# Performance work log

Measured on AMD Instinct MI355X. Metric: run time of the kernel, lower is better.

The kernel has to match this reference:

```python
import jax, jax.numpy as jnp
import numpy as np


def quat2mat(q):
    # q: [B,4] in (w,x,y,z) order; normalize then standard rotation matrix.
    q = q / jnp.linalg.norm(q, axis=-1, keepdims=True)
    w, x, y, z = q[:, 0], q[:, 1], q[:, 2], q[:, 3]
    R = jnp.stack([
        1 - 2 * (y * y + z * z), 2 * (x * y - w * z), 2 * (x * z + w * y),
        2 * (x * y + w * z), 1 - 2 * (x * x + z * z), 2 * (y * z - w * x),
        2 * (x * z - w * y), 2 * (y * z + w * x), 1 - 2 * (x * x + y * y),
    ], axis=-1).reshape(-1, 3, 3)
    return R


def setup_inputs() -> dict:
    key = jax.random.key(0)
    k1, k2, k3, k4, k5 = jax.random.split(key, 5)
    B, N = 32, 2048
    return {
        "q_est": jax.random.normal(k1, (B, 4), dtype=jnp.float32),
        "q_gt": jax.random.normal(k2, (B, 4), dtype=jnp.float32),
        "T": jax.random.normal(k3, (B, 3), dtype=jnp.float32),
        "pts": jax.random.normal(k4, (B, N, 3), dtype=jnp.float32),
        "symmetries": jax.random.randint(k5, (B, 1), 0, 2, dtype=jnp.int32),
    }


def reference(q_est, q_gt, T, pts, symmetries):
    # ego=False path: T unused.
    B = pts.shape[0]
    N = pts.shape[1]
    sym = symmetries.reshape(-1).astype(bool)  # [B]

    R_est = quat2mat(q_est)  # [B,3,3]
    R_gt = quat2mat(q_gt)

    pts_t = jnp.transpose(pts, (0, 2, 1))        # [B,3,N]
    pts_est = R_est @ pts_t                       # [B,3,N]
    pts_gt = R_gt @ pts_t                         # [B,3,N]

    # PLoss per-point squared distances: [B,N]
    d_p = jnp.sum((pts_est - pts_gt) ** 2, axis=1)

    # SLoss: pairwise squared dists via bmm decomposition, then min over gt points.
    x = jnp.transpose(pts_est, (0, 2, 1))  # [B,N,3]
    y = jnp.transpose(pts_gt, (0, 2, 1))   # [B,N,3]
    xx = jnp.sum(x * x, axis=-1)           # [B,N] (diag of x x^T)
    yy = jnp.sum(y * y, axis=-1)           # [B,N]
    zz = jnp.einsum('bnd,bmd->bnm', x, y)  # [B,N,N]
    P = xx[:, :, None] + yy[:, None, :] - 2.0 * zz
    d_s = jnp.min(P, axis=2)               # [B,N]

    # num_sym * s_loss / size + num_non_sym * p_loss / size simplifies to
    # (masked_sum_s + masked_sum_p) / (2 * N * B); num_sym/num_non_sym cancel.
    sum_s = jnp.sum(jnp.where(sym[:, None], d_s, 0.0))
    sum_p = jnp.sum(jnp.where(sym[:, None], 0.0, d_p))
    return (sum_s + sum_p) / (2.0 * N * B)
```

## Files before the change

### kernel.cpp

```cpp
#include <hip/hip_runtime.h>


#define NPTS  2048
#define NC    16
#define TPB   128
#define YPT   (NPTS / TPB)

static_assert(NPTS / NC == TPB, "one x-point per thread");

__device__ __forceinline__ void quat2mat(const float* __restrict__ q, float R[9]) {
    float w = q[0], x = q[1], y = q[2], z = q[3];
    float inv = 1.0f / sqrtf(w*w + x*x + y*y + z*z);
    w *= inv; x *= inv; y *= inv; z *= inv;
    R[0] = 1.f - 2.f*(y*y + z*z); R[1] = 2.f*(x*y - w*z);       R[2] = 2.f*(x*z + w*y);
    R[3] = 2.f*(x*y + w*z);       R[4] = 1.f - 2.f*(x*x + z*z); R[5] = 2.f*(y*z - w*x);
    R[6] = 2.f*(x*z - w*y);       R[7] = 2.f*(y*z + w*x);       R[8] = 1.f - 2.f*(x*x + y*y);
}

__device__ __forceinline__ float block_reduce_add(float v, float* red) {
    #pragma unroll
    for (int off = 32; off > 0; off >>= 1)
        v += __shfl_down(v, off, 64);
    const int tid = threadIdx.x;
    if ((tid & 63) == 0) red[tid >> 6] = v;
    __syncthreads();
    return red[0] + red[1];
}

__global__ __launch_bounds__(TPB) void pts_loss_fused(
    const float* __restrict__ q_est, const float* __restrict__ q_gt,
    const float* __restrict__ pts, const int* __restrict__ symmetries,
    float* __restrict__ out, float scale)
{
    const int b   = blockIdx.x;
    const int c   = blockIdx.y;
    const int tid = threadIdx.x;

    __shared__ float4 ybuf[NPTS];
    __shared__ float  red[TPB / 64];

    const bool is_sym = symmetries[b] != 0;
    const float* pb = pts + (size_t)b * NPTS * 3;

    float Re[9], Rg[9];
    quat2mat(q_est + 4*b, Re);
    quat2mat(q_gt  + 4*b, Rg);

    const int   n  = c * TPB + tid;
    const float p0 = pb[3*n+0], p1 = pb[3*n+1], p2 = pb[3*n+2];

    float s;
    if (!is_sym) {
        float d0 = (Re[0]-Rg[0])*p0 + (Re[1]-Rg[1])*p1 + (Re[2]-Rg[2])*p2;
        float d1 = (Re[3]-Rg[3])*p0 + (Re[4]-Rg[4])*p1 + (Re[5]-Rg[5])*p2;
        float d2 = (Re[6]-Rg[6])*p0 + (Re[7]-Rg[7])*p1 + (Re[8]-Rg[8])*p2;
        s = d0*d0 + d1*d1 + d2*d2;
    } else {
        #pragma unroll
        for (int k = 0; k < YPT; ++k) {
            int m = k * TPB + tid;
            float a0 = pb[3*m+0], a1 = pb[3*m+1], a2 = pb[3*m+2];
            float y0 = Rg[0]*a0 + Rg[1]*a1 + Rg[2]*a2;
            float y1 = Rg[3]*a0 + Rg[4]*a1 + Rg[5]*a2;
            float y2 = Rg[6]*a0 + Rg[7]*a1 + Rg[8]*a2;
            ybuf[m] = make_float4(y0, y1, y2, y0*y0 + y1*y1 + y2*y2);
        }
        __syncthreads();

        float x0 = Re[0]*p0 + Re[1]*p1 + Re[2]*p2;
        float x1 = Re[3]*p0 + Re[4]*p1 + Re[5]*p2;
        float x2 = Re[6]*p0 + Re[7]*p1 + Re[8]*p2;
        float nx0 = -2.f*x0, nx1 = -2.f*x1, nx2 = -2.f*x2;
        float xx  = x0*x0 + x1*x1 + x2*x2;

        float m0 = 1e30f, m1 = 1e30f, m2 = 1e30f, m3 = 1e30f;
        #pragma unroll 2
        for (int m = 0; m < NPTS; m += 4) {
            float4 ya = ybuf[m+0];
            float4 yb = ybuf[m+1];
            float4 yc = ybuf[m+2];
            float4 yd = ybuf[m+3];
            m0 = fminf(m0, fmaf(nx0, ya.x, fmaf(nx1, ya.y, fmaf(nx2, ya.z, ya.w))));
            m1 = fminf(m1, fmaf(nx0, yb.x, fmaf(nx1, yb.y, fmaf(nx2, yb.z, yb.w))));
            m2 = fminf(m2, fmaf(nx0, yc.x, fmaf(nx1, yc.y, fmaf(nx2, yc.z, yc.w))));
            m3 = fminf(m3, fmaf(nx0, yd.x, fmaf(nx1, yd.y, fmaf(nx2, yd.z, yd.w))));
        }
        s = xx + fminf(fminf(m0, m1), fminf(m2, m3));
    }

    s = block_reduce_add(s, red);
    if (tid == 0) atomicAdd(out, s * scale);
}

extern "C" void kernel_launch(void* const* d_in, const int* in_sizes, int n_in,
                              void* d_out, int out_size, void* d_ws, size_t ws_size,
                              hipStream_t stream) {
    const float* q_est = (const float*)d_in[0];
    const float* q_gt  = (const float*)d_in[1];
    const float* pts   = (const float*)d_in[3];
    const int*   sym   = (const int*)d_in[4];
    float* out = (float*)d_out;

    const int B = in_sizes[0] / 4;
    const float scale = 1.0f / (2.0f * (float)NPTS * (float)B);

    hipMemsetAsync(out, 0, sizeof(float), stream);
    dim3 grid(B, NC);
    pts_loss_fused<<<grid, TPB, 0, stream>>>(q_est, q_gt, pts, sym, out, scale);
}
```

Measured before the change: 92.44 us.

## Split gt-point range across waves and merge nearest-neighbor minima via shared atomicMin

Measured after the change: 77.85 us. -15.8%, faster.

```diff
diff --git a/kernel.cpp b/kernel.cpp
--- a/kernel.cpp
+++ b/kernel.cpp
@@ -2,11 +2,13 @@
 
 
 #define NPTS  2048
-#define NC    16
-#define TPB   128
-#define YPT   (NPTS / TPB)
-
-static_assert(NPTS / NC == TPB, "one x-point per thread");
+#define TPB   512
+#define NW    (TPB / 64)
+#define PX    2
+#define CHUNK (64 * PX)
+#define NCX   (NPTS / CHUNK)
+#define MR    (NPTS / NW)
+#define SPT   (NPTS / TPB)
 
 __device__ __forceinline__ void quat2mat(const float* __restrict__ q, float R[9]) {
     float w = q[0], x = q[1], y = q[2], z = q[3];
@@ -17,6 +19,15 @@
     R[6] = 2.f*(x*z - w*y);       R[7] = 2.f*(y*z + w*x);       R[8] = 1.f - 2.f*(x*x + y*y);
 }
 
+__device__ __forceinline__ unsigned fenc(float f) {
+    unsigned u = __float_as_uint(f);
+    return u ^ (unsigned)(((int)u >> 31) | 0x80000000);
+}
+__device__ __forceinline__ float fdec(unsigned e) {
+    unsigned u = (e & 0x80000000u) ? (e ^ 0x80000000u) : ~e;
+    return __uint_as_float(u);
+}
+
 __device__ __forceinline__ float block_reduce_add(float v, float* red) {
     #pragma unroll
     for (int off = 32; off > 0; off >>= 1)
@@ -24,20 +35,26 @@
     const int tid = threadIdx.x;
     if ((tid & 63) == 0) red[tid >> 6] = v;
     __syncthreads();
-    return red[0] + red[1];
+    float s = 0.f;
+    #pragma unroll
+    for (int w = 0; w < NW; ++w) s += red[w];
+    return s;
 }
 
-__global__ __launch_bounds__(TPB) void pts_loss_fused(
+__global__ __launch_bounds__(TPB) void pts_loss(
     const float* __restrict__ q_est, const float* __restrict__ q_gt,
     const float* __restrict__ pts, const int* __restrict__ symmetries,
     float* __restrict__ out, float scale)
 {
-    const int b   = blockIdx.x;
-    const int c   = blockIdx.y;
-    const int tid = threadIdx.x;
+    const int b    = blockIdx.x;
+    const int c    = blockIdx.y;
+    const int tid  = threadIdx.x;
+    const int lane = tid & 63;
+    const int w    = tid >> 6;
 
-    __shared__ float4 ybuf[NPTS];
-    __shared__ float  red[TPB / 64];
+    __shared__ float4   ybuf[NPTS];
+    __shared__ unsigned dmin[CHUNK];
+    __shared__ float    red[NW];
 
     const bool is_sym = symmetries[b] != 0;
     const float* pb = pts + (size_t)b * NPTS * 3;
@@ -46,48 +63,64 @@
     quat2mat(q_est + 4*b, Re);
     quat2mat(q_gt  + 4*b, Rg);
 
-    const int   n  = c * TPB + tid;
-    const float p0 = pb[3*n+0], p1 = pb[3*n+1], p2 = pb[3*n+2];
+    if (!is_sym) {
+        float s = 0.f;
+        if (tid < CHUNK) {
+            int n = c * CHUNK + tid;
+            float p0 = pb[3*n+0], p1 = pb[3*n+1], p2 = pb[3*n+2];
+            float d0 = (Re[0]-Rg[0])*p0 + (Re[1]-Rg[1])*p1 + (Re[2]-Rg[2])*p2;
+            float d1 = (Re[3]-Rg[3])*p0 + (Re[4]-Rg[4])*p1 + (Re[5]-Rg[5])*p2;
+            float d2 = (Re[6]-Rg[6])*p0 + (Re[7]-Rg[7])*p1 + (Re[8]-Rg[8])*p2;
+            s = d0*d0 + d1*d1 + d2*d2;
+        }
+        s = block_reduce_add(s, red);
+        if (tid == 0) atomicAdd(out, s * scale);
+        return;
+    }
 
-    float s;
-    if (!is_sym) {
-        float d0 = (Re[0]-Rg[0])*p0 + (Re[1]-Rg[1])*p1 + (Re[2]-Rg[2])*p2;
-        float d1 = (Re[3]-Rg[3])*p0 + (Re[4]-Rg[4])*p1 + (Re[5]-Rg[5])*p2;
-        float d2 = (Re[6]-Rg[6])*p0 + (Re[7]-Rg[7])*p1 + (Re[8]-Rg[8])*p2;
-        s = d0*d0 + d1*d1 + d2*d2;
-    } else {
-        #pragma unroll
-        for (int k = 0; k < YPT; ++k) {
-            int m = k * TPB + tid;
-            float a0 = pb[3*m+0], a1 = pb[3*m+1], a2 = pb[3*m+2];
-            float y0 = Rg[0]*a0 + Rg[1]*a1 + Rg[2]*a2;
-            float y1 = Rg[3]*a0 + Rg[4]*a1 + Rg[5]*a2;
-            float y2 = Rg[6]*a0 + Rg[7]*a1 + Rg[8]*a2;
-            ybuf[m] = make_float4(y0, y1, y2, y0*y0 + y1*y1 + y2*y2);
-        }
-        __syncthreads();
+    if (tid < CHUNK) dmin[tid] = 0xFFFFFFFFu;
 
+    #pragma unroll
+    for (int j = 0; j < SPT; ++j) {
+        int m = j * TPB + tid;
+        float a0 = pb[3*m+0], a1 = pb[3*m+1], a2 = pb[3*m+2];
+        float y0 = Rg[0]*a0 + Rg[1]*a1 + Rg[2]*a2;
+        float y1 = Rg[3]*a0 + Rg[4]*a1 + Rg[5]*a2;
+        float y2 = Rg[6]*a0 + Rg[7]*a1 + Rg[8]*a2;
+        ybuf[m] = make_float4(y0, y1, y2, y0*y0 + y1*y1 + y2*y2);
+    }
+    __syncthreads();
+
+    float nx0[PX], nx1[PX], nx2[PX], xx[PX], mins[PX];
+    #pragma unroll
+    for (int k = 0; k < PX; ++k) {
+        int n = c * CHUNK + k * 64 + lane;
+        float p0 = pb[3*n+0], p1 = pb[3*n+1], p2 = pb[3*n+2];
         float x0 = Re[0]*p0 + Re[1]*p1 + Re[2]*p2;
         float x1 = Re[3]*p0 + Re[4]*p1 + Re[5]*p2;
         float x2 = Re[6]*p0 + Re[7]*p1 + Re[8]*p2;
-        float nx0 = -2.f*x0, nx1 = -2.f*x1, nx2 = -2.f*x2;
-        float xx  = x0*x0 + x1*x1 + x2*x2;
-
-        float m0 = 1e30f, m1 = 1e30f, m2 = 1e30f, m3 = 1e30f;
-        #pragma unroll 2
-        for (int m = 0; m < NPTS; m += 4) {
-            float4 ya = ybuf[m+0];
-            float4 yb = ybuf[m+1];
-            float4 yc = ybuf[m+2];
-            float4 yd = ybuf[m+3];
-            m0 = fminf(m0, fmaf(nx0, ya.x, fmaf(nx1, ya.y, fmaf(nx2, ya.z, ya.w))));
-            m1 = fminf(m1, fmaf(nx0, yb.x, fmaf(nx1, yb.y, fmaf(nx2, yb.z, yb.w))));
-            m2 = fminf(m2, fmaf(nx0, yc.x, fmaf(nx1, yc.y, fmaf(nx2, yc.z, yc.w))));
-            m3 = fminf(m3, fmaf(nx0, yd.x, fmaf(nx1, yd.y, fmaf(nx2, yd.z, yd.w))));
-        }
-        s = xx + fminf(fminf(m0, m1), fminf(m2, m3));
+        nx0[k] = -2.f*x0; nx1[k] = -2.f*x1; nx2[k] = -2.f*x2;
+        xx[k]  = x0*x0 + x1*x1 + x2*x2;
+        mins[k] = 1e30f;
     }
 
+    const int mbase = w * MR;
+    #pragma unroll 4
+    for (int i = 0; i < MR; ++i) {
+        float4 y = ybuf[mbase + i];
+        #pragma unroll
+        for (int k = 0; k < PX; ++k) {
+            float t = fmaf(nx0[k], y.x, fmaf(nx1[k], y.y, fmaf(nx2[k], y.z, y.w)));
+            mins[k] = fminf(mins[k], t);
+        }
+    }
+
+    #pragma unroll
+    for (int k = 0; k < PX; ++k)
+        atomicMin(&dmin[k * 64 + lane], fenc(mins[k] + xx[k]));
+    __syncthreads();
+
+    float s = (tid < CHUNK) ? fdec(dmin[tid]) : 0.f;
     s = block_reduce_add(s, red);
     if (tid == 0) atomicAdd(out, s * scale);
 }
@@ -105,6 +138,6 @@
     const float scale = 1.0f / (2.0f * (float)NPTS * (float)B);
 
     hipMemsetAsync(out, 0, sizeof(float), stream);
-    dim3 grid(B, NC);
-    pts_loss_fused<<<grid, TPB, 0, stream>>>(q_est, q_gt, pts, sym, out, scale);
+    dim3 grid(B, NCX);
+    pts_loss<<<grid, TPB, 0, stream>>>(q_est, q_gt, pts, sym, out, scale);
 }
```
